# Kernel optimization log

Measured on AMD Instinct MI355X. Metric: run time of the kernel, lower is better.

The kernel has to match this reference:

```python
import jax, jax.numpy as jnp
import numpy as np
import math

N_HEAD = 16
H_DIM = 32            # per-half head dim
LAMBDA_INIT = 0.8 - 0.6 * math.exp(-0.3 * 1)  # depth = 1
EPS = 1e-6


def _rmsnorm(x, scale):
    xf = x.astype(jnp.float32)
    normed = xf * jax.lax.rsqrt(jnp.mean(xf * xf, axis=-1, keepdims=True) + EPS)
    return normed.astype(x.dtype) * scale


def setup_inputs() -> dict:
    key = jax.random.key(0)
    ks = jax.random.split(key, 8)
    B, T, D = 2, 2048, 1024
    return {
        "x": jax.random.normal(ks[0], (B, T, D), jnp.float32),
        "Wqkv": jax.random.normal(ks[1], (D, 3 * D), jnp.float32) * (1.0 / math.sqrt(D)),
        "Wproj": jax.random.normal(ks[2], (D, D), jnp.float32) * (1.0 / math.sqrt(D)),
        "lambda_q1": jax.random.normal(ks[3], (H_DIM,), jnp.float32) * 0.1,
        "lambda_k1": jax.random.normal(ks[4], (H_DIM,), jnp.float32) * 0.1,
        "lambda_q2": jax.random.normal(ks[5], (H_DIM,), jnp.float32) * 0.1,
        "lambda_k2": jax.random.normal(ks[6], (H_DIM,), jnp.float32) * 0.1,
        "rms_scale": jnp.ones((2 * H_DIM,), jnp.float32),
    }


def reference(x, Wqkv, Wproj, lambda_q1, lambda_k1, lambda_q2, lambda_k2, rms_scale):
    B, T, C = x.shape
    H, h = N_HEAD, H_DIM
    qkv = x @ Wqkv                          # [B,T,3C]
    q, k, v = jnp.split(qkv, 3, axis=-1)
    q = q.reshape(B, T, 2 * H, h).transpose(0, 2, 1, 3)   # [B,2H,T,h]
    k = k.reshape(B, T, 2 * H, h).transpose(0, 2, 1, 3)   # [B,2H,T,h]
    v = v.reshape(B, T, H, 2 * h).transpose(0, 2, 1, 3)   # [B,H,T,2h]
    q1, q2 = jnp.split(q, 2, axis=1)        # each [B,H,T,h]
    k1, k2 = jnp.split(k, 2, axis=1)
    scale = 1.0 / math.sqrt(h)

    def sdpa(qh, kh):
        scores = jnp.einsum('bhqd,bhkd->bhqk', qh, kh) * scale
        return jnp.einsum('bhqk,bhkd->bhqd', jax.nn.softmax(scores, axis=-1), v)

    attn1 = sdpa(q1, k1)                    # [B,H,T,2h]
    attn2 = sdpa(q2, k2)
    lam1 = jnp.exp(jnp.sum(lambda_q1 * lambda_k1))
    lam2 = jnp.exp(jnp.sum(lambda_q2 * lambda_k2))
    lam = lam1 - lam2 + LAMBDA_INIT
    out = attn1 - lam * attn2
    out = _rmsnorm(out, rms_scale) * (1.0 - LAMBDA_INIT)
    out = out.transpose(0, 2, 1, 3).reshape(B, T, C)
    return out @ Wproj
```

## Files before the change

### kernel.cpp

```cpp
#include <hip/hip_runtime.h>
#include <cstdint>
#include <cstddef>


typedef short bf16x8 __attribute__((ext_vector_type(8)));
typedef float f32x4  __attribute__((ext_vector_type(4)));
typedef float f32x16 __attribute__((ext_vector_type(16)));
typedef unsigned short u16;
typedef u16 u16x4v __attribute__((ext_vector_type(4)));
typedef unsigned int u32;
typedef u32 u32x2 __attribute__((ext_vector_type(2)));
typedef u32 u32x4 __attribute__((ext_vector_type(4)));

#define LAMBDA_INIT 0.35550906759096926f
#define ONE_MINUS_LAMBDA_INIT 0.6444909324090307f
#define SCORE_SCALE 0.17677669529663687f

__device__ __forceinline__ u16 f2bf(float f) {
  uint32_t u = __float_as_uint(f);
  u += 0x7fffu + ((u >> 16) & 1u);
  return (u16)(u >> 16);
}

__device__ __forceinline__ void gload_lds16(const void* g, void* lds) {
  __builtin_amdgcn_global_load_lds(
      (const __attribute__((address_space(1))) void*)g,
      (__attribute__((address_space(3))) void*)lds, 16, 0, 0);
}

__device__ __forceinline__ u32 cvtpk_bf16(float lo, float hi) {
  u32 r;
  asm("v_cvt_pk_bf16_f32 %0, %1, %2" : "=v"(r) : "v"(lo), "v"(hi));
  return r;
}

__device__ __forceinline__ float xchg32f(float v, int hi) {
  u32x2 r = __builtin_amdgcn_permlane32_swap(__float_as_uint(v), __float_as_uint(v), false, false);
  return __uint_as_float(hi ? r.x : r.y);
}

__device__ __forceinline__ float rmax16(const f32x16& v) {
  float m = v[0];
#pragma unroll
  for (int i = 1; i < 16; ++i) m = fmaxf(m, v[i]);
  return m;
}

__device__ __forceinline__ float rsum16(const f32x16& v) {
  float a = 0.f;
#pragma unroll
  for (int i = 0; i < 16; ++i) a += v[i];
  return a;
}

__global__ void conv_x_kernel(const float* __restrict__ in, u16* __restrict__ out, int n4) {
  int i = blockIdx.x * blockDim.x + threadIdx.x;
  if (i < n4) {
    float4 v = ((const float4*)in)[i];
    u16x4v o;
    o.x = f2bf(v.x); o.y = f2bf(v.y); o.z = f2bf(v.z); o.w = f2bf(v.w);
    ((u16x4v*)out)[i] = o;
  }
}

__global__ void conv_transpose_kernel(const float* __restrict__ W, u16* __restrict__ WT,
                                      int K, int N) {
  __shared__ u16 L[64][72];
  const int n0 = blockIdx.x * 64, k0 = blockIdx.y * 64;
#pragma unroll
  for (int i = 0; i < 16; ++i) {
    int lin = i * 256 + threadIdx.x;
    int rr = lin >> 6, cc = lin & 63;
    L[rr][cc] = f2bf(W[(size_t)(k0 + rr) * N + n0 + cc]);
  }
  __syncthreads();
#pragma unroll
  for (int i = 0; i < 16; ++i) {
    int lin = i * 256 + threadIdx.x;
    int rr = lin >> 6, cc = lin & 63;
    WT[(size_t)(n0 + rr) * K + k0 + cc] = L[cc][rr];
  }
}

template <typename OutT>
__global__ __launch_bounds__(256, 2) void gemm_bt(const u16* __restrict__ A,
                                                  const u16* __restrict__ Bt,
                                                  OutT* __restrict__ C,
                                                  int M, int N, int K) {
  __shared__ __align__(16) u16 As[2][128 * 32];
  __shared__ __align__(16) u16 Bs[2][128 * 32];
  const int wid = threadIdx.x >> 6, lane = threadIdx.x & 63;
  const int l15 = lane & 15, lhi = lane >> 4;
  const int wm = wid >> 1, wn = wid & 1;
  const int tm = blockIdx.x * 128, tn = blockIdx.y * 128;
  const int rr = lane >> 2, cb = (lane & 3) * 8;
  const int nkt = K >> 5;

  f32x4 acc[4][4];
#pragma unroll
  for (int m = 0; m < 4; ++m)
#pragma unroll
    for (int n = 0; n < 4; ++n) acc[m][n] = (f32x4){0.f, 0.f, 0.f, 0.f};

  auto stage = [&](int buf, int kt) {
#pragma unroll
    for (int i = 0; i < 2; ++i) {
      int lr = wid * 32 + i * 16;
      gload_lds16(A + (size_t)(tm + lr + rr) * K + kt * 32 + cb, &As[buf][lr * 32]);
      gload_lds16(Bt + (size_t)(tn + lr + rr) * K + kt * 32 + cb, &Bs[buf][lr * 32]);
    }
  };

  stage(0, 0);
  __syncthreads();
  int buf = 0;
  for (int kt = 0; kt < nkt; ++kt) {
    if (kt + 1 < nkt) stage(buf ^ 1, kt + 1);
    bf16x8 af[4], bfr[4];
#pragma unroll
    for (int m = 0; m < 4; ++m)
      af[m] = *(const bf16x8*)&As[buf][(wm * 64 + m * 16 + l15) * 32 + lhi * 8];
#pragma unroll
    for (int n = 0; n < 4; ++n)
      bfr[n] = *(const bf16x8*)&Bs[buf][(wn * 64 + n * 16 + l15) * 32 + lhi * 8];
#pragma unroll
    for (int m = 0; m < 4; ++m)
#pragma unroll
      for (int n = 0; n < 4; ++n)
        acc[m][n] = __builtin_amdgcn_mfma_f32_16x16x32_bf16(af[m], bfr[n], acc[m][n], 0, 0, 0);
    __syncthreads();
    buf ^= 1;
  }

#pragma unroll
  for (int m = 0; m < 4; ++m)
#pragma unroll
    for (int n = 0; n < 4; ++n)
#pragma unroll
      for (int r = 0; r < 4; ++r) {
        int row = tm + wm * 64 + m * 16 + lhi * 4 + r;
        int col = tn + wn * 64 + n * 16 + l15;
        float v = acc[m][n][r];
        if constexpr (sizeof(OutT) == 2)
          C[(size_t)row * N + col] = (OutT)f2bf(v);
        else
          C[(size_t)row * N + col] = v;
      }
}

#define KLD 32
#define VLD 72

__global__ __launch_bounds__(256, 2) void diff_attn_kernel(
    const u16* __restrict__ qkv,
    const float* __restrict__ lq1, const float* __restrict__ lk1,
    const float* __restrict__ lq2, const float* __restrict__ lk2,
    const float* __restrict__ rms_scale,
    u16* __restrict__ y) {
  __shared__ __align__(16) u16 K1s[64 * KLD];
  __shared__ __align__(16) u16 K2s[64 * KLD];
  __shared__ __align__(16) u16 VTs[64 * VLD];

  const int tid = threadIdx.x;
  const int wid = tid >> 6, lane = tid & 63;
  const int l31 = lane & 31, hi = lane >> 5;

  const int id = blockIdx.x;
  const int swz = (id & 7) * 64 + (id >> 3);
  const int qt = swz & 15;
  const int bh = swz >> 4;
  const int b = bh >> 4, head = bh & 15;
  const size_t row0 = (size_t)b * 2048;

  float d1 = 0.f, d2 = 0.f;
#pragma unroll
  for (int i = 0; i < 32; ++i) { d1 += lq1[i] * lk1[i]; d2 += lq2[i] * lk2[i]; }
  const float lam = expf(d1) - expf(d2) + LAMBDA_INIT;

  const int qrow = qt * 128 + wid * 32 + l31;
  const u16* qrp = qkv + (row0 + qrow) * 3072;
  bf16x8 q1f[2], q2f[2];
#pragma unroll
  for (int c = 0; c < 2; ++c) {
    q1f[c] = *(const bf16x8*)(qrp + head * 32 + c * 16 + hi * 8);
    q2f[c] = *(const bf16x8*)(qrp + 512 + head * 32 + c * 16 + hi * 8);
  }

  f32x16 o1[2], o2[2];
#pragma unroll
  for (int dt = 0; dt < 2; ++dt)
#pragma unroll
    for (int i = 0; i < 16; ++i) { o1[dt][i] = 0.f; o2[dt][i] = 0.f; }
  float m1 = -1e30f, m2 = -1e30f;
  float ls1 = 0.f, ls2 = 0.f;

  auto process = [&](const bf16x8* qf, const u16* Ks, const bf16x8 (*vf)[2][2],
                     float& m, float& ls, f32x16* o) {
    f32x16 s[2];
#pragma unroll
    for (int t = 0; t < 2; ++t) {
#pragma unroll
      for (int i = 0; i < 16; ++i) s[t][i] = 0.f;
      const int row = t * 32 + l31;
      const int sg = 8 * ((row >> 1) & 3);
#pragma unroll
      for (int c = 0; c < 2; ++c) {
        bf16x8 kf = *(const bf16x8*)&Ks[row * KLD + ((c * 16 + hi * 8) ^ sg)];
        s[t] = __builtin_amdgcn_mfma_f32_32x32x16_bf16(kf, qf[c], s[t], 0, 0, 0);
      }
    }
    float pm = fmaxf(rmax16(s[0]), rmax16(s[1]));
    pm = fmaxf(pm, xchg32f(pm, hi));
    if (!__all(pm - m <= 8.0f)) {
      float mn = fmaxf(m, pm);
      float corr = __expf((m - mn) * SCORE_SCALE);
      m = mn;
      ls *= corr;
#pragma unroll
      for (int dt = 0; dt < 2; ++dt)
#pragma unroll
        for (int i = 0; i < 16; ++i) o[dt][i] *= corr;
    }
#pragma unroll
    for (int t = 0; t < 2; ++t)
#pragma unroll
      for (int i = 0; i < 16; ++i)
        s[t][i] = __expf((s[t][i] - m) * SCORE_SCALE);
    ls += rsum16(s[0]) + rsum16(s[1]);
#pragma unroll
    for (int t = 0; t < 2; ++t) {
      u32 W[4][2];
#pragma unroll
      for (int g = 0; g < 4; ++g)
#pragma unroll
        for (int u = 0; u < 2; ++u)
          W[g][u] = cvtpk_bf16(s[t][4 * g + 2 * u], s[t][4 * g + 2 * u + 1]);
#pragma unroll
      for (int kap = 0; kap < 2; ++kap) {
        u32x2 r0 = __builtin_amdgcn_permlane32_swap(W[2 * kap][0], W[2 * kap + 1][0], false, false);
        u32x2 r1 = __builtin_amdgcn_permlane32_swap(W[2 * kap][1], W[2 * kap + 1][1], false, false);
        u32x4 words = {r0.x, r1.x, r0.y, r1.y};
        bf16x8 pB = __builtin_bit_cast(bf16x8, words);
#pragma unroll
        for (int dt = 0; dt < 2; ++dt)
          o[dt] = __builtin_amdgcn_mfma_f32_32x32x16_bf16(vf[t][kap][dt], pB, o[dt], 0, 0, 0);
      }
    }
  };

  for (int kt = 0; kt < 32; ++kt) {
    const size_t krow0 = row0 + kt * 64;
    {
      const int srow = wid * 16 + (lane >> 2);
      const int gcol = 8 * ((lane & 3) ^ ((lane >> 3) & 3));
      const u16* g = qkv + (krow0 + srow) * 3072 + 1024 + head * 32 + gcol;
      gload_lds16(g, &K1s[wid * 512]);
      gload_lds16(g + 512, &K2s[wid * 512]);
    }
    {
#pragma unroll
      for (int h2 = 0; h2 < 2; ++h2) {
        int vid = h2 * 256 + tid;
        int vrow = vid >> 3, d0 = (vid & 7) * 8;
        bf16x8 vv = *(const bf16x8*)(qkv + (krow0 + vrow) * 3072 + 2048 + head * 64 + d0);
        int wrow = vrow ^ (d0 & 56);
#pragma unroll
        for (int e = 0; e < 8; ++e) VTs[(d0 + e) * VLD + wrow] = (u16)vv[e];
      }
    }
    __syncthreads();

    bf16x8 vf[2][2][2];
#pragma unroll
    for (int t = 0; t < 2; ++t)
#pragma unroll
      for (int kap = 0; kap < 2; ++kap)
#pragma unroll
        for (int dt = 0; dt < 2; ++dt) {
          int d = dt * 32 + l31;
          int koff = (t * 32 + kap * 16 + hi * 8) ^ ((d & 56));
          vf[t][kap][dt] = *(const bf16x8*)&VTs[d * VLD + koff];
        }

    process(q1f, K1s, vf, m1, ls1, o1);
    process(q2f, K2s, vf, m2, ls2, o2);
    __syncthreads();
  }

  ls1 += xchg32f(ls1, hi);
  ls2 += xchg32f(ls2, hi);
  const float il1 = 1.0f / ls1, il2 = 1.0f / ls2;

  f32x16 v[2];
  float ssq = 0.f;
#pragma unroll
  for (int dt = 0; dt < 2; ++dt)
#pragma unroll
    for (int i = 0; i < 16; ++i) {
      float a = o1[dt][i] * il1 - lam * (o2[dt][i] * il2);
      v[dt][i] = a;
      ssq += a * a;
    }
  ssq += xchg32f(ssq, hi);
  const float inv = rsqrtf(ssq * (1.0f / 64.0f) + 1e-6f);

  u16* yr = y + (row0 + qrow) * 1024 + head * 64;
#pragma unroll
  for (int dt = 0; dt < 2; ++dt)
#pragma unroll
    for (int rg = 0; rg < 4; ++rg) {
      int dbase = 8 * rg + 4 * hi + 32 * dt;
      u16x4v w;
#pragma unroll
      for (int bb = 0; bb < 4; ++bb)
        w[bb] = f2bf(v[dt][4 * rg + bb] * inv * rms_scale[dbase + bb] * ONE_MINUS_LAMBDA_INIT);
      *(u16x4v*)(yr + dbase) = w;
    }
}

extern "C" void kernel_launch(void* const* d_in, const int* in_sizes, int n_in,
                              void* d_out, int out_size, void* d_ws, size_t ws_size,
                              hipStream_t stream) {
  const float* x     = (const float*)d_in[0];
  const float* Wqkv  = (const float*)d_in[1];
  const float* Wproj = (const float*)d_in[2];
  const float* lq1   = (const float*)d_in[3];
  const float* lk1   = (const float*)d_in[4];
  const float* lq2   = (const float*)d_in[5];
  const float* lk2   = (const float*)d_in[6];
  const float* rms   = (const float*)d_in[7];
  float* out = (float*)d_out;

  char* ws = (char*)d_ws;
  u16* xb     = (u16*)(ws);
  u16* WqkvT  = (u16*)(ws + (size_t)(8  << 20));
  u16* WprojT = (u16*)(ws + (size_t)(14 << 20));
  u16* qkvb   = (u16*)(ws + (size_t)(16 << 20));
  u16* yb     = xb;

  conv_x_kernel<<<4096, 256, 0, stream>>>(x, xb, 1048576);
  conv_transpose_kernel<<<dim3(48, 16), 256, 0, stream>>>(Wqkv, WqkvT, 1024, 3072);
  conv_transpose_kernel<<<dim3(16, 16), 256, 0, stream>>>(Wproj, WprojT, 1024, 1024);
  gemm_bt<u16><<<dim3(32, 24), 256, 0, stream>>>(xb, WqkvT, qkvb, 4096, 3072, 1024);
  diff_attn_kernel<<<512, 256, 0, stream>>>(qkvb, lq1, lk1, lq2, lk2, rms, yb);
  gemm_bt<float><<<dim3(32, 8), 256, 0, stream>>>(yb, WprojT, out, 4096, 1024, 1024);
}
```

Before: 242.4 us.

## Double-buffer K/V tiles in diff-attention loop to overlap loads with compute

Adds a second LDS buffer for K1, K2 and transposed V, prefetching the next key tile (async global-to-LDS for K, register staging for V) while the current tile is processed. One of the two barriers per iteration is removed. The aim is to hide global memory latency behind the MFMA work. In exchange, shared memory use doubles and V staging registers are added, which may reduce occupancy under the 2-blocks launch bound.

```diff
diff --git a/kernel.cpp b/kernel.cpp
--- a/kernel.cpp
+++ b/kernel.cpp
@@ -157,9 +157,9 @@
     const float* __restrict__ lq2, const float* __restrict__ lk2,
     const float* __restrict__ rms_scale,
     u16* __restrict__ y) {
-  __shared__ __align__(16) u16 K1s[64 * KLD];
-  __shared__ __align__(16) u16 K2s[64 * KLD];
-  __shared__ __align__(16) u16 VTs[64 * VLD];
+  __shared__ __align__(16) u16 K1s[2][64 * KLD];
+  __shared__ __align__(16) u16 K2s[2][64 * KLD];
+  __shared__ __align__(16) u16 VTs[2][64 * VLD];
 
   const int tid = threadIdx.x;
   const int wid = tid >> 6, lane = tid & 63;
@@ -193,6 +193,34 @@
     for (int i = 0; i < 16; ++i) { o1[dt][i] = 0.f; o2[dt][i] = 0.f; }
   float m1 = -1e30f, m2 = -1e30f;
   float ls1 = 0.f, ls2 = 0.f;
+
+  auto issueK = [&](int buf, int kt) {
+    const size_t krow0 = row0 + (size_t)kt * 64;
+    const int srow = wid * 16 + (lane >> 2);
+    const int gcol = 8 * ((lane & 3) ^ ((lane >> 3) & 3));
+    const u16* g = qkv + (krow0 + srow) * 3072 + 1024 + head * 32 + gcol;
+    gload_lds16(g, &K1s[buf][wid * 512]);
+    gload_lds16(g + 512, &K2s[buf][wid * 512]);
+  };
+  auto loadV = [&](int kt, bf16x8* nv) {
+    const size_t krow0 = row0 + (size_t)kt * 64;
+#pragma unroll
+    for (int h2 = 0; h2 < 2; ++h2) {
+      int vid = h2 * 256 + tid;
+      int vrow = vid >> 3, d0 = (vid & 7) * 8;
+      nv[h2] = *(const bf16x8*)(qkv + (krow0 + vrow) * 3072 + 2048 + head * 64 + d0);
+    }
+  };
+  auto writeV = [&](int buf, const bf16x8* nv) {
+#pragma unroll
+    for (int h2 = 0; h2 < 2; ++h2) {
+      int vid = h2 * 256 + tid;
+      int vrow = vid >> 3, d0 = (vid & 7) * 8;
+      int wrow = vrow ^ (d0 & 56);
+#pragma unroll
+      for (int e = 0; e < 8; ++e) VTs[buf][(d0 + e) * VLD + wrow] = (u16)nv[h2][e];
+    }
+  };
 
   auto process = [&](const bf16x8* qf, const u16* Ks, const bf16x8 (*vf)[2][2],
                      float& m, float& ls, f32x16* o) {
@@ -248,27 +276,18 @@
     }
   };
 
+  {
+    bf16x8 v0[2];
+    issueK(0, 0);
+    loadV(0, v0);
+    writeV(0, v0);
+  }
+  __syncthreads();
+
+  int buf = 0;
   for (int kt = 0; kt < 32; ++kt) {
-    const size_t krow0 = row0 + kt * 64;
-    {
-      const int srow = wid * 16 + (lane >> 2);
-      const int gcol = 8 * ((lane & 3) ^ ((lane >> 3) & 3));
-      const u16* g = qkv + (krow0 + srow) * 3072 + 1024 + head * 32 + gcol;
-      gload_lds16(g, &K1s[wid * 512]);
-      gload_lds16(g + 512, &K2s[wid * 512]);
-    }
-    {
-#pragma unroll
-      for (int h2 = 0; h2 < 2; ++h2) {
-        int vid = h2 * 256 + tid;
-        int vrow = vid >> 3, d0 = (vid & 7) * 8;
-        bf16x8 vv = *(const bf16x8*)(qkv + (krow0 + vrow) * 3072 + 2048 + head * 64 + d0);
-        int wrow = vrow ^ (d0 & 56);
-#pragma unroll
-        for (int e = 0; e < 8; ++e) VTs[(d0 + e) * VLD + wrow] = (u16)vv[e];
-      }
-    }
-    __syncthreads();
+    bf16x8 nv[2];
+    if (kt + 1 < 32) { issueK(buf ^ 1, kt + 1); loadV(kt + 1, nv); }
 
     bf16x8 vf[2][2][2];
 #pragma unroll
@@ -278,13 +297,16 @@
 #pragma unroll
         for (int dt = 0; dt < 2; ++dt) {
           int d = dt * 32 + l31;
-          int koff = (t * 32 + kap * 16 + hi * 8) ^ ((d & 56));
-          vf[t][kap][dt] = *(const bf16x8*)&VTs[d * VLD + koff];
+          int koff = (t * 32 + kap * 16 + hi * 8) ^ (d & 56);
+          vf[t][kap][dt] = *(const bf16x8*)&VTs[buf][d * VLD + koff];
         }
 
-    process(q1f, K1s, vf, m1, ls1, o1);
-    process(q2f, K2s, vf, m2, ls2, o2);
+    process(q1f, &K1s[buf][0], vf, m1, ls1, o1);
+    process(q2f, &K2s[buf][0], vf, m2, ls2, o2);
+
+    if (kt + 1 < 32) writeV(buf ^ 1, nv);
     __syncthreads();
+    buf ^= 1;
   }
 
   ls1 += xchg32f(ls1, hi);
```

After: 243.5 us. Within noise of the previous version (+0.5%).
